# Kernel tuning notes

Hardware: AMD Instinct MI355X
Metric: run time of the kernel (lower is better)

Reference implementation:

```python
import jax, jax.numpy as jnp
import numpy as np

HEADS = 4
NEG_SLOPE = 0.2  # PyG GATConv default
LN_EPS = 1e-5


def setup_inputs() -> dict:
    key = jax.random.key(0)
    ks = jax.random.split(key, 12)
    N, D, E = 30000, 128, 480000
    s = 1.0 / np.sqrt(D)
    return {
        "x": jax.random.normal(ks[0], (N, D), dtype=jnp.float32),
        "edge_index": jax.random.randint(ks[1], (2, E), 0, N, dtype=jnp.int64),
        "W_gat": jax.random.normal(ks[2], (HEADS, D, D), dtype=jnp.float32) * s,
        "att_src": jax.random.normal(ks[3], (HEADS, D), dtype=jnp.float32) * s,
        "att_dst": jax.random.normal(ks[4], (HEADS, D), dtype=jnp.float32) * s,
        "b_gat": jnp.zeros((D,), dtype=jnp.float32),
        "W_gcn": jax.random.normal(ks[5], (D, D), dtype=jnp.float32) * s,
        "b_gcn": jnp.zeros((D,), dtype=jnp.float32),
        "W_gate": jax.random.normal(ks[6], (2 * D, 2), dtype=jnp.float32) * (1.0 / np.sqrt(2 * D)),
        "b_gate": jnp.zeros((2,), dtype=jnp.float32),
        "gamma": jnp.ones((D,), dtype=jnp.float32),
        "beta": jnp.zeros((D,), dtype=jnp.float32),
    }


def reference(x, edge_index, W_gat, att_src, att_dst, b_gat, W_gcn, b_gcn,
              W_gate, b_gate, gamma, beta):
    N, D = x.shape
    # Both PyG GATConv and GCNConv add self-loops by default.
    loops = jnp.arange(N, dtype=edge_index.dtype)
    src = jnp.concatenate([edge_index[0], loops])  # message source j
    dst = jnp.concatenate([edge_index[1], loops])  # message target i

    # ---- GATConv (heads=4, concat=False -> mean over heads), eval (no dropout) ----
    xh = jnp.einsum('nd,hdf->nhf', x, W_gat)            # [N, H, D]
    a_s = jnp.einsum('nhf,hf->nh', xh, att_src)         # [N, H]
    a_d = jnp.einsum('nhf,hf->nh', xh, att_dst)         # [N, H]
    e = jax.nn.leaky_relu(a_s[src] + a_d[dst], NEG_SLOPE)  # [E', H]
    # segment softmax over incoming edges of each destination node
    m = jax.ops.segment_max(e, dst, num_segments=N)     # every node has a self-loop
    alpha = jnp.exp(e - m[dst])
    denom = jax.ops.segment_sum(alpha, dst, num_segments=N)
    alpha = alpha / denom[dst]                          # [E', H]
    # aggregate per head (fixed small loop keeps peak memory at E*D per head)
    gat_acc = jnp.zeros((N, D), dtype=x.dtype)
    for h in range(HEADS):
        msg = alpha[:, h:h + 1] * xh[:, h, :][src]      # [E', D]
        gat_acc = gat_acc + jax.ops.segment_sum(msg, dst, num_segments=N)
    gat_out = gat_acc / HEADS + b_gat

    xg = x @ W_gcn                                      # [N, D]
    deg = jax.ops.segment_sum(jnp.ones_like(src, dtype=x.dtype), dst, num_segments=N)
    dinv = jnp.where(deg > 0, jax.lax.rsqrt(deg), 0.0)
    coef = dinv[src] * dinv[dst]                        # [E']
    gcn_out = jax.ops.segment_sum(coef[:, None] * xg[src], dst, num_segments=N) + b_gcn

    # ---- gated fusion + residual + LayerNorm ----
    gate = jax.nn.softmax(jnp.concatenate([gat_out, gcn_out], axis=-1) @ W_gate + b_gate, axis=-1)
    fused = gate[:, 0:1] * gat_out + gate[:, 1:2] * gcn_out
    h = fused + gat_out
    mu = jnp.mean(h, axis=-1, keepdims=True)
    var = jnp.mean((h - mu) ** 2, axis=-1, keepdims=True)
    return (h - mu) * jax.lax.rsqrt(var + LN_EPS) * gamma + beta
```

## Files before the change

kernel.cpp:

```cpp
#include <hip/hip_runtime.h>
#include <hip/hip_bf16.h>

#define D 128
#define NH 4
#define NEG_SLOPE 0.2f
#define LN_EPS 1e-5f

typedef __attribute__((ext_vector_type(4))) float f32x4;
typedef __attribute__((ext_vector_type(8))) short bf16x8;

__device__ __forceinline__ float bf2f(unsigned short u) {
  union { unsigned int i; float f; } c; c.i = ((unsigned int)u) << 16; return c.f;
}
__device__ __forceinline__ unsigned short f2bf(float f) {
  union { float f; unsigned int i; } c; c.f = f;
  unsigned int r = c.i + 0x7FFFu + ((c.i >> 16) & 1u);
  return (unsigned short)(r >> 16);
}

__global__ __launch_bounds__(128) void k_prep(
    const float* __restrict__ Wgat, const float* __restrict__ Wgcn,
    const float* __restrict__ att_src, const float* __restrict__ att_dst,
    unsigned short* __restrict__ Wt2g, unsigned short* __restrict__ Wt2c,
    float* __restrict__ wtil_s, float* __restrict__ wtil_d)
{
  int c = blockIdx.x, t = threadIdx.x;
  if (c < 128) {
    #pragma unroll
    for (int i = 0; i < 4; ++i) {
      int k = t + i * 128;
      int h = k >> 7, kk = k & 127;
      Wt2g[c * 512 + k] = f2bf(Wgat[((size_t)h * D + kk) * D + c]);
    }
  } else if (c < 256) {
    int cc = c - 128;
    Wt2c[cc * 128 + t] = f2bf(Wgcn[(size_t)t * D + cc]);
  } else {
    int b2 = c - 256;
    int h = b2 >> 1, which = b2 & 1;
    const float* av = (which ? att_dst : att_src) + h * D;
    const float* Wrow = Wgat + ((size_t)h * D + t) * D;
    float s = 0.f;
    for (int f = 0; f < D; ++f) s += Wrow[f] * av[f];
    (which ? wtil_d : wtil_s)[h * D + t] = s;
  }
}

__global__ __launch_bounds__(256) void k_xb(
    const float* __restrict__ x,
    const float* __restrict__ wtil_s, const float* __restrict__ wtil_d,
    unsigned short* __restrict__ xb, float* __restrict__ a_s, float* __restrict__ a_d,
    int* __restrict__ deg, int N)
{
  const int w = threadIdx.x >> 6, l = threadIdx.x & 63;
  const int n = blockIdx.x * 4 + w;
  if (n >= N) return;
  if (l == 0) deg[n] = 0;
  float2 xv = ((const float2*)(x + (size_t)n * D))[l];
  ushort2 p; p.x = f2bf(xv.x); p.y = f2bf(xv.y);
  *(ushort2*)(xb + (size_t)n * D + 2 * l) = p;
  float s0 = xv.x * wtil_s[2*l]       + xv.y * wtil_s[2*l+1];
  float s1 = xv.x * wtil_s[D+2*l]     + xv.y * wtil_s[D+2*l+1];
  float s2 = xv.x * wtil_s[2*D+2*l]   + xv.y * wtil_s[2*D+2*l+1];
  float s3 = xv.x * wtil_s[3*D+2*l]   + xv.y * wtil_s[3*D+2*l+1];
  float d0 = xv.x * wtil_d[2*l]       + xv.y * wtil_d[2*l+1];
  float d1 = xv.x * wtil_d[D+2*l]     + xv.y * wtil_d[D+2*l+1];
  float d2 = xv.x * wtil_d[2*D+2*l]   + xv.y * wtil_d[2*D+2*l+1];
  float d3 = xv.x * wtil_d[3*D+2*l]   + xv.y * wtil_d[3*D+2*l+1];
  #pragma unroll
  for (int off = 32; off; off >>= 1) {
    s0 += __shfl_xor(s0, off); s1 += __shfl_xor(s1, off);
    s2 += __shfl_xor(s2, off); s3 += __shfl_xor(s3, off);
    d0 += __shfl_xor(d0, off); d1 += __shfl_xor(d1, off);
    d2 += __shfl_xor(d2, off); d3 += __shfl_xor(d3, off);
  }
  if (l == 0) {
    ((float4*)a_s)[n] = make_float4(s0, s1, s2, s3);
    ((float4*)a_d)[n] = make_float4(d0, d1, d2, d3);
  }
}

__global__ void k_deg(const int* __restrict__ ei, int E, int N, int* __restrict__ deg)
{
  int e = blockIdx.x * blockDim.x + threadIdx.x;
  if (e >= E + N) return;
  int dst = (e < E) ? ei[E + e] : (e - E);
  atomicAdd(&deg[dst], 1);
}

__global__ void k_scan1(const int* __restrict__ deg, int N, int* __restrict__ bsum)
{
  __shared__ int s[256];
  int t = threadIdx.x;
  int i = blockIdx.x * 256 + t;
  s[t] = (i < N) ? deg[i] : 0;
  __syncthreads();
  for (int off = 128; off; off >>= 1) {
    if (t < off) s[t] += s[t + off];
    __syncthreads();
  }
  if (t == 0) bsum[blockIdx.x] = s[0];
}

__global__ void k_scan2(int* __restrict__ bsum, int nb)
{
  __shared__ int s[128];
  int t = threadIdx.x;
  int v = (t < nb) ? bsum[t] : 0;
  s[t] = v; __syncthreads();
  for (int off = 1; off < 128; off <<= 1) {
    int xv = (t >= off) ? s[t - off] : 0;
    __syncthreads();
    s[t] += xv;
    __syncthreads();
  }
  if (t < nb) bsum[t] = s[t] - v;
}

__global__ void k_scan3(const int* __restrict__ deg, const int* __restrict__ bsum,
                        int N, int Et, int* __restrict__ row_ptr,
                        int* __restrict__ cursor, float* __restrict__ dinv)
{
  __shared__ int s[256];
  int t = threadIdx.x;
  int i = blockIdx.x * 256 + t;
  int v = (i < N) ? deg[i] : 0;
  s[t] = v; __syncthreads();
  for (int off = 1; off < 256; off <<= 1) {
    int xv = (t >= off) ? s[t - off] : 0;
    __syncthreads();
    s[t] += xv;
    __syncthreads();
  }
  if (i < N) {
    int excl = s[t] - v + bsum[blockIdx.x];
    row_ptr[i] = excl;
    cursor[i] = excl;
    dinv[i] = rsqrtf((float)v);
  }
  if (i == 0) row_ptr[N] = Et;
}

__global__ void k_fill(const int* __restrict__ ei, int E, int N,
                       int* __restrict__ cursor, int* __restrict__ col_src)
{
  int e = blockIdx.x * blockDim.x + threadIdx.x;
  if (e >= E + N) return;
  int src, dst;
  if (e < E) { src = ei[e]; dst = ei[E + e]; }
  else       { src = e - E; dst = src; }
  int pos = atomicAdd(&cursor[dst], 1);
  col_src[pos] = src;
}

__global__ __launch_bounds__(256) void k_agg2(
    const unsigned short* __restrict__ xb,
    const float* __restrict__ a_s, const float* __restrict__ a_d,
    const int* __restrict__ row_ptr, const int* __restrict__ col_src,
    const float* __restrict__ dinv,
    unsigned short* __restrict__ UV, int N)
{
  __shared__ float4 sh_al[8][33];
  __shared__ int    sh_src[8][33];
  __shared__ float  sh_cf[8][33];
  const int hw = threadIdx.x >> 5, lh = threadIdx.x & 31;
  const int n = blockIdx.x * 8 + hw;
  if (n >= N) return;
  const int start = row_ptr[n], end = row_ptr[n + 1];
  const float4 adn = ((const float4*)a_d)[n];

  float den0 = 0.f, den1 = 0.f, den2 = 0.f, den3 = 0.f;
  float ug[4][4] = {};
  float vg[4] = {};

  for (int base = start; base < end; base += 32) {
    const int cnt = min(32, end - base);
    if (lh < cnt) {
      int s = col_src[base + lh];
      float4 as4 = ((const float4*)a_s)[s];
      float e0 = as4.x + adn.x; e0 = (e0 >= 0.f) ? e0 : NEG_SLOPE * e0;
      float e1 = as4.y + adn.y; e1 = (e1 >= 0.f) ? e1 : NEG_SLOPE * e1;
      float e2 = as4.z + adn.z; e2 = (e2 >= 0.f) ? e2 : NEG_SLOPE * e2;
      float e3 = as4.w + adn.w; e3 = (e3 >= 0.f) ? e3 : NEG_SLOPE * e3;
      float x0 = __expf(e0), x1 = __expf(e1), x2 = __expf(e2), x3 = __expf(e3);
      den0 += x0; den1 += x1; den2 += x2; den3 += x3;
      sh_al[hw][lh] = make_float4(x0, x1, x2, x3);
      sh_src[hw][lh] = s;
      sh_cf[hw][lh] = dinv[s];
    }
    if (lh == 0) {
      sh_al[hw][cnt] = make_float4(0.f, 0.f, 0.f, 0.f);
      sh_src[hw][cnt] = 0;
      sh_cf[hw][cnt] = 0.f;
    }
    for (int j = 0; j < cnt; j += 2) {
      float4 alA = sh_al[hw][j];     int sA = sh_src[hw][j];     float cfA = sh_cf[hw][j];
      float4 alB = sh_al[hw][j + 1]; int sB = sh_src[hw][j + 1]; float cfB = sh_cf[hw][j + 1];
      ushort4 xA = *(const ushort4*)(xb + ((size_t)sA << 7) + (lh << 2));
      ushort4 xB = *(const ushort4*)(xb + ((size_t)sB << 7) + (lh << 2));
      float fa[4] = {bf2f(xA.x), bf2f(xA.y), bf2f(xA.z), bf2f(xA.w)};
      float fb[4] = {bf2f(xB.x), bf2f(xB.y), bf2f(xB.z), bf2f(xB.w)};
      float aA[4] = {alA.x, alA.y, alA.z, alA.w};
      float aB[4] = {alB.x, alB.y, alB.z, alB.w};
      #pragma unroll
      for (int h = 0; h < 4; ++h)
        #pragma unroll
        for (int d = 0; d < 4; ++d)
          ug[h][d] += aA[h] * fa[d] + aB[h] * fb[d];
      #pragma unroll
      for (int d = 0; d < 4; ++d)
        vg[d] += cfA * fa[d] + cfB * fb[d];
    }
  }

  #pragma unroll
  for (int off = 16; off; off >>= 1) {
    den0 += __shfl_xor(den0, off); den1 += __shfl_xor(den1, off);
    den2 += __shfl_xor(den2, off); den3 += __shfl_xor(den3, off);
  }
  const float r[4] = {1.f / den0, 1.f / den1, 1.f / den2, 1.f / den3};
  const float dn = dinv[n];
  unsigned short* uvp = UV + (size_t)n * 640;
  #pragma unroll
  for (int h = 0; h < 4; ++h) {
    ushort4 u;
    u.x = f2bf(ug[h][0] * r[h]); u.y = f2bf(ug[h][1] * r[h]);
    u.z = f2bf(ug[h][2] * r[h]); u.w = f2bf(ug[h][3] * r[h]);
    *(ushort4*)(uvp + h * 128 + 4 * lh) = u;
  }
  ushort4 v4;
  v4.x = f2bf(vg[0] * dn); v4.y = f2bf(vg[1] * dn);
  v4.z = f2bf(vg[2] * dn); v4.w = f2bf(vg[3] * dn);
  *(ushort4*)(uvp + 512 + 4 * lh) = v4;
}

__global__ __launch_bounds__(256) void k_gemm3(
    const unsigned short* __restrict__ UV,
    const unsigned short* __restrict__ Wt2g, const unsigned short* __restrict__ Wt2c,
    const float* __restrict__ b_gat, const float* __restrict__ b_gcn,
    const float* __restrict__ W_gate, const float* __restrict__ b_gate,
    const float* __restrict__ gamma, const float* __restrict__ beta,
    float* __restrict__ out, int N)
{
  __shared__ unsigned short As[128 * 128];
  __shared__ unsigned short Bs[128 * 128];
  __shared__ float ec[8][128];
  const int t = threadIdx.x;
  const int m0 = blockIdx.x * 128;

  {
    int idx = t * 4;
    #pragma unroll
    for (int i = 0; i < 4; ++i) {
      int arr = (idx + i) >> 7, c = (idx + i) & 127;
      float v;
      switch (arr) {
        case 0: v = b_gat[c]; break;
        case 1: v = b_gcn[c]; break;
        case 2: v = W_gate[2 * c]; break;
        case 3: v = W_gate[2 * c + 1]; break;
        case 4: v = W_gate[256 + 2 * c]; break;
        case 5: v = W_gate[256 + 2 * c + 1]; break;
        case 6: v = gamma[c]; break;
        default: v = beta[c]; break;
      }
      ec[arr][c] = v;
    }
  }

  const int w = t >> 6, l = t & 63;
  const int lrow = l & 15, lk = l >> 4;

  f32x4 accg[2][8], accc[2][8];
  #pragma unroll
  for (int m = 0; m < 2; ++m)
    #pragma unroll
    for (int n = 0; n < 8; ++n) {
      accg[m][n] = (f32x4){0.f, 0.f, 0.f, 0.f};
      accc[m][n] = (f32x4){0.f, 0.f, 0.f, 0.f};
    }

  for (int kc = 0; kc < 5; ++kc) {
    const int abase = (kc < 4) ? kc * 128 : 512;
    __syncthreads();
    #pragma unroll
    for (int i = 0; i < 8; ++i) {
      int g = i * 256 + t;
      int row = g >> 4, kb = g & 15;
      int gr = m0 + row;
      uint4 v = make_uint4(0u, 0u, 0u, 0u);
      if (gr < N) v = *(const uint4*)(UV + (size_t)gr * 640 + abase + kb * 8);
      *(uint4*)&As[row * 128 + ((kb ^ (row & 7)) << 3)] = v;
    }
    #pragma unroll
    for (int i = 0; i < 8; ++i) {
      int g = i * 256 + t;
      int col = g >> 4, kb = g & 15;
      uint4 v = (kc < 4)
        ? *(const uint4*)(Wt2g + (size_t)col * 512 + kc * 128 + kb * 8)
        : *(const uint4*)(Wt2c + (size_t)col * 128 + kb * 8);
      *(uint4*)&Bs[col * 128 + ((kb ^ (col & 7)) << 3)] = v;
    }
    __syncthreads();
    if (kc < 4) {
      #pragma unroll
      for (int ks = 0; ks < 4; ++ks) {
        int kb = ks * 4 + lk;
        bf16x8 a[2], b[8];
        #pragma unroll
        for (int m = 0; m < 2; ++m) {
          int row = w * 32 + m * 16 + lrow;
          a[m] = *(const bf16x8*)&As[row * 128 + ((kb ^ (row & 7)) << 3)];
        }
        #pragma unroll
        for (int n = 0; n < 8; ++n) {
          int col = n * 16 + lrow;
          b[n] = *(const bf16x8*)&Bs[col * 128 + ((kb ^ (col & 7)) << 3)];
        }
        #pragma unroll
        for (int m = 0; m < 2; ++m)
          #pragma unroll
          for (int n = 0; n < 8; ++n)
            accg[m][n] = __builtin_amdgcn_mfma_f32_16x16x32_bf16(a[m], b[n], accg[m][n], 0, 0, 0);
      }
    } else {
      #pragma unroll
      for (int ks = 0; ks < 4; ++ks) {
        int kb = ks * 4 + lk;
        bf16x8 a[2], b[8];
        #pragma unroll
        for (int m = 0; m < 2; ++m) {
          int row = w * 32 + m * 16 + lrow;
          a[m] = *(const bf16x8*)&As[row * 128 + ((kb ^ (row & 7)) << 3)];
        }
        #pragma unroll
        for (int n = 0; n < 8; ++n) {
          int col = n * 16 + lrow;
          b[n] = *(const bf16x8*)&Bs[col * 128 + ((kb ^ (col & 7)) << 3)];
        }
        #pragma unroll
        for (int m = 0; m < 2; ++m)
          #pragma unroll
          for (int n = 0; n < 8; ++n)
            accc[m][n] = __builtin_amdgcn_mfma_f32_16x16x32_bf16(a[m], b[n], accc[m][n], 0, 0, 0);
      }
    }
  }

  const float bg0 = b_gate[0], bg1 = b_gate[1];
  #pragma unroll
  for (int m = 0; m < 2; ++m) {
    #pragma unroll
    for (int j = 0; j < 4; ++j) {
      const int r = m0 + w * 32 + m * 16 + lk * 4 + j;
      float ga[8], gc[8];
      float z0 = 0.f, z1 = 0.f;
      #pragma unroll
      for (int n = 0; n < 8; ++n) {
        int c = n * 16 + lrow;
        ga[n] = accg[m][n][j] * 0.25f + ec[0][c];
        gc[n] = accc[m][n][j] + ec[1][c];
        z0 += ga[n] * ec[2][c] + gc[n] * ec[4][c];
        z1 += ga[n] * ec[3][c] + gc[n] * ec[5][c];
      }
      #pragma unroll
      for (int off = 8; off; off >>= 1) { z0 += __shfl_xor(z0, off); z1 += __shfl_xor(z1, off); }
      z0 += bg0; z1 += bg1;
      float mz = fmaxf(z0, z1);
      float e0 = __expf(z0 - mz), e1 = __expf(z1 - mz);
      float inv = 1.f / (e0 + e1);
      float w0 = e0 * inv, w1 = e1 * inv;
      float h[8], ss = 0.f;
      #pragma unroll
      for (int n = 0; n < 8; ++n) { h[n] = (1.f + w0) * ga[n] + w1 * gc[n]; ss += h[n]; }
      #pragma unroll
      for (int off = 8; off; off >>= 1) ss += __shfl_xor(ss, off);
      float mu = ss * (1.f / 128.f);
      float vs = 0.f;
      #pragma unroll
      for (int n = 0; n < 8; ++n) { h[n] -= mu; vs += h[n] * h[n]; }
      #pragma unroll
      for (int off = 8; off; off >>= 1) vs += __shfl_xor(vs, off);
      float rstd = rsqrtf(vs * (1.f / 128.f) + LN_EPS);
      if (r < N) {
        #pragma unroll
        for (int n = 0; n < 8; ++n) {
          int c = n * 16 + lrow;
          out[(size_t)r * 128 + c] = h[n] * rstd * ec[6][c] + ec[7][c];
        }
      }
    }
  }
}

extern "C" void kernel_launch(void* const* d_in, const int* in_sizes, int n_in,
                              void* d_out, int out_size, void* d_ws, size_t ws_size,
                              hipStream_t stream)
{
  const float* x       = (const float*)d_in[0];
  const int*   ei      = (const int*)d_in[1];
  const float* Wgat    = (const float*)d_in[2];
  const float* att_src = (const float*)d_in[3];
  const float* att_dst = (const float*)d_in[4];
  const float* b_gat   = (const float*)d_in[5];
  const float* Wgcn    = (const float*)d_in[6];
  const float* b_gcn   = (const float*)d_in[7];
  const float* W_gate  = (const float*)d_in[8];
  const float* b_gate  = (const float*)d_in[9];
  const float* gamma   = (const float*)d_in[10];
  const float* beta    = (const float*)d_in[11];
  float* out = (float*)d_out;

  const int N  = in_sizes[0] / D;
  const int E  = in_sizes[1] / 2;
  const int Et = E + N;

  char* p = (char*)d_ws;
  unsigned short* xb   = (unsigned short*)p; p += (size_t)N * D * 2;
  unsigned short* UV   = (unsigned short*)p; p += (size_t)N * 640 * 2;
  unsigned short* Wt2g = (unsigned short*)p; p += (size_t)128 * 512 * 2;
  unsigned short* Wt2c = (unsigned short*)p; p += (size_t)128 * 128 * 2;
  float* wtil_s  = (float*)p; p += 512 * 4;
  float* wtil_d  = (float*)p; p += 512 * 4;
  float* a_s     = (float*)p; p += (size_t)N * NH * 4;
  float* a_d     = (float*)p; p += (size_t)N * NH * 4;
  float* dinv    = (float*)p; p += (size_t)N * 4;
  int* deg       = (int*)p;   p += (size_t)N * 4;
  int* row_ptr   = (int*)p;   p += (size_t)(N + 1) * 4;
  int* cursor    = (int*)p;   p += (size_t)N * 4;
  int* col_src   = (int*)p;   p += (size_t)Et * 4;
  int* bsum      = (int*)p;   p += 1024;

  k_prep<<<264, 128, 0, stream>>>(Wgat, Wgcn, att_src, att_dst,
                                   Wt2g, Wt2c, wtil_s, wtil_d);
  k_xb<<<(N + 3) / 4, 256, 0, stream>>>(x, wtil_s, wtil_d, xb, a_s, a_d, deg, N);
  k_deg<<<(Et + 255) / 256, 256, 0, stream>>>(ei, E, N, deg);
  int nb = (N + 255) / 256;
  k_scan1<<<nb, 256, 0, stream>>>(deg, N, bsum);
  k_scan2<<<1, 128, 0, stream>>>(bsum, nb);
  k_scan3<<<nb, 256, 0, stream>>>(deg, bsum, N, Et, row_ptr, cursor, dinv);
  k_fill<<<(Et + 255) / 256, 256, 0, stream>>>(ei, E, N, cursor, col_src);
  k_agg2<<<(N + 7) / 8, 256, 0, stream>>>(xb, a_s, a_d, row_ptr, col_src, dinv, UV, N);
  k_gemm3<<<(N + 127) / 128, 256, 0, stream>>>(UV, Wt2g, Wt2c, b_gat, b_gcn,
                                                W_gate, b_gate, gamma, beta, out, N);
  (void)n_in; (void)out_size; (void)ws_size;
}
```

Measured before the change: 145.4 us.

## Merge degree count into node kernel and halve GEMM row tile

```diff
diff --git a/kernel.cpp b/kernel.cpp
--- a/kernel.cpp
+++ b/kernel.cpp
@@ -22,7 +22,8 @@
     const float* __restrict__ Wgat, const float* __restrict__ Wgcn,
     const float* __restrict__ att_src, const float* __restrict__ att_dst,
     unsigned short* __restrict__ Wt2g, unsigned short* __restrict__ Wt2c,
-    float* __restrict__ wtil_s, float* __restrict__ wtil_d)
+    float* __restrict__ wtil_s, float* __restrict__ wtil_d,
+    int* __restrict__ deg, int N)
 {
   int c = blockIdx.x, t = threadIdx.x;
   if (c < 128) {
@@ -35,7 +36,7 @@
   } else if (c < 256) {
     int cc = c - 128;
     Wt2c[cc * 128 + t] = f2bf(Wgcn[(size_t)t * D + cc]);
-  } else {
+  } else if (c < 264) {
     int b2 = c - 256;
     int h = b2 >> 1, which = b2 & 1;
     const float* av = (which ? att_dst : att_src) + h * D;
@@ -43,19 +44,30 @@
     float s = 0.f;
     for (int f = 0; f < D; ++f) s += Wrow[f] * av[f];
     (which ? wtil_d : wtil_s)[h * D + t] = s;
-  }
-}
-
-__global__ __launch_bounds__(256) void k_xb(
+  } else {
+    int i = (c - 264) * 128 + t;
+    if (i < N) deg[i] = 0;
+  }
+}
+
+__global__ __launch_bounds__(256) void k_xb_deg(
     const float* __restrict__ x,
     const float* __restrict__ wtil_s, const float* __restrict__ wtil_d,
     unsigned short* __restrict__ xb, float* __restrict__ a_s, float* __restrict__ a_d,
-    int* __restrict__ deg, int N)
-{
+    const int* __restrict__ ei, int* __restrict__ deg,
+    int N, int E, int NBN)
+{
+  if ((int)blockIdx.x >= NBN) {
+    int e = (blockIdx.x - NBN) * 256 + threadIdx.x;
+    if (e < E + N) {
+      int dst = (e < E) ? ei[E + e] : (e - E);
+      atomicAdd(&deg[dst], 1);
+    }
+    return;
+  }
   const int w = threadIdx.x >> 6, l = threadIdx.x & 63;
   const int n = blockIdx.x * 4 + w;
   if (n >= N) return;
-  if (l == 0) deg[n] = 0;
   float2 xv = ((const float2*)(x + (size_t)n * D))[l];
   ushort2 p; p.x = f2bf(xv.x); p.y = f2bf(xv.y);
   *(ushort2*)(xb + (size_t)n * D + 2 * l) = p;
@@ -80,14 +92,6 @@
   }
 }
 
-__global__ void k_deg(const int* __restrict__ ei, int E, int N, int* __restrict__ deg)
-{
-  int e = blockIdx.x * blockDim.x + threadIdx.x;
-  if (e >= E + N) return;
-  int dst = (e < E) ? ei[E + e] : (e - E);
-  atomicAdd(&deg[dst], 1);
-}
-
 __global__ void k_scan1(const int* __restrict__ deg, int N, int* __restrict__ bsum)
 {
   __shared__ int s[256];
@@ -242,11 +246,11 @@
     const float* __restrict__ gamma, const float* __restrict__ beta,
     float* __restrict__ out, int N)
 {
-  __shared__ unsigned short As[128 * 128];
+  __shared__ unsigned short As[64 * 128];
   __shared__ unsigned short Bs[128 * 128];
   __shared__ float ec[8][128];
   const int t = threadIdx.x;
-  const int m0 = blockIdx.x * 128;
+  const int m0 = blockIdx.x * 64;
 
   {
     int idx = t * 4;
@@ -270,21 +274,20 @@
 
   const int w = t >> 6, l = t & 63;
   const int lrow = l & 15, lk = l >> 4;
-
-  f32x4 accg[2][8], accc[2][8];
+  const int arow = w * 16 + lrow;
+
+  f32x4 accg[8], accc[8];
   #pragma unroll
-  for (int m = 0; m < 2; ++m)
-    #pragma unroll
-    for (int n = 0; n < 8; ++n) {
-      accg[m][n] = (f32x4){0.f, 0.f, 0.f, 0.f};
-      accc[m][n] = (f32x4){0.f, 0.f, 0.f, 0.f};
-    }
+  for (int n = 0; n < 8; ++n) {
+    accg[n] = (f32x4){0.f, 0.f, 0.f, 0.f};
+    accc[n] = (f32x4){0.f, 0.f, 0.f, 0.f};
+  }
 
   for (int kc = 0; kc < 5; ++kc) {
     const int abase = (kc < 4) ? kc * 128 : 512;
     __syncthreads();
     #pragma unroll
-    for (int i = 0; i < 8; ++i) {
+    for (int i = 0; i < 4; ++i) {
       int g = i * 256 + t;
       int row = g >> 4, kb = g & 15;
       int gr = m0 + row;
@@ -302,92 +305,58 @@
       *(uint4*)&Bs[col * 128 + ((kb ^ (col & 7)) << 3)] = v;
     }
     __syncthreads();
-    if (kc < 4) {
+    f32x4* acc = (kc < 4) ? accg : accc;
+    #pragma unroll
+    for (int ks = 0; ks < 4; ++ks) {
+      int kb = ks * 4 + lk;
+      bf16x8 a = *(const bf16x8*)&As[arow * 128 + ((kb ^ (arow & 7)) << 3)];
       #pragma unroll
-      for (int ks = 0; ks < 4; ++ks) {
-        int kb = ks * 4 + lk;
-        bf16x8 a[2], b[8];
-        #pragma unroll
-        for (int m = 0; m < 2; ++m) {
-          int row = w * 32 + m * 16 + lrow;
-          a[m] = *(const bf16x8*)&As[row * 128 + ((kb ^ (row & 7)) << 3)];
-        }
-        #pragma unroll
-        for (int n = 0; n < 8; ++n) {
-          int col = n * 16 + lrow;
-          b[n] = *(const bf16x8*)&Bs[col * 128 + ((kb ^ (col & 7)) << 3)];
-        }
-        #pragma unroll
-        for (int m = 0; m < 2; ++m)
-          #pragma unroll
-          for (int n = 0; n < 8; ++n)
-            accg[m][n] = __builtin_amdgcn_mfma_f32_16x16x32_bf16(a[m], b[n], accg[m][n], 0, 0, 0);
-      }
-    } else {
-      #pragma unroll
-      for (int ks = 0; ks < 4; ++ks) {
-        int kb = ks * 4 + lk;
-        bf16x8 a[2], b[8];
-        #pragma unroll
-        for (int m = 0; m < 2; ++m) {
-          int row = w * 32 + m * 16 + lrow;
-          a[m] = *(const bf16x8*)&As[row * 128 + ((kb ^ (row & 7)) << 3)];
-        }
-        #pragma unroll
-        for (int n = 0; n < 8; ++n) {
-          int col = n * 16 + lrow;
-          b[n] = *(const bf16x8*)&Bs[col * 128 + ((kb ^ (col & 7)) << 3)];
-        }
-        #pragma unroll
-        for (int m = 0; m < 2; ++m)
-          #pragma unroll
-          for (int n = 0; n < 8; ++n)
-            accc[m][n] = __builtin_amdgcn_mfma_f32_16x16x32_bf16(a[m], b[n], accc[m][n], 0, 0, 0);
+      for (int n = 0; n < 8; ++n) {
+        int col = n * 16 + lrow;
+        bf16x8 b = *(const bf16x8*)&Bs[col * 128 + ((kb ^ (col & 7)) << 3)];
+        acc[n] = __builtin_amdgcn_mfma_f32_16x16x32_bf16(a, b, acc[n], 0, 0, 0);
       }
     }
   }
 
   const float bg0 = b_gate[0], bg1 = b_gate[1];
   #pragma unroll
-  for (int m = 0; m < 2; ++m) {
-    #pragma unroll
-    for (int j = 0; j < 4; ++j) {
-      const int r = m0 + w * 32 + m * 16 + lk * 4 + j;
-      float ga[8], gc[8];
-      float z0 = 0.f, z1 = 0.f;
+  for (int j = 0; j < 4; ++j) {
+    const int r = m0 + w * 16 + lk * 4 + j;
+    float ga[8], gc[8];
+    float z0 = 0.f, z1 = 0.f;
+    #pragma unroll
+    for (int n = 0; n < 8; ++n) {
+      int c = n * 16 + lrow;
+      ga[n] = accg[n][j] * 0.25f + ec[0][c];
+      gc[n] = accc[n][j] + ec[1][c];
+      z0 += ga[n] * ec[2][c] + gc[n] * ec[4][c];
+      z1 += ga[n] * ec[3][c] + gc[n] * ec[5][c];
+    }
+    #pragma unroll
+    for (int off = 8; off; off >>= 1) { z0 += __shfl_xor(z0, off); z1 += __shfl_xor(z1, off); }
+    z0 += bg0; z1 += bg1;
+    float mz = fmaxf(z0, z1);
+    float e0 = __expf(z0 - mz), e1 = __expf(z1 - mz);
+    float inv = 1.f / (e0 + e1);
+    float w0 = e0 * inv, w1 = e1 * inv;
+    float h[8], ss = 0.f;
+    #pragma unroll
+    for (int n = 0; n < 8; ++n) { h[n] = (1.f + w0) * ga[n] + w1 * gc[n]; ss += h[n]; }
+    #pragma unroll
+    for (int off = 8; off; off >>= 1) ss += __shfl_xor(ss, off);
+    float mu = ss * (1.f / 128.f);
+    float vs = 0.f;
+    #pragma unroll
+    for (int n = 0; n < 8; ++n) { h[n] -= mu; vs += h[n] * h[n]; }
+    #pragma unroll
+    for (int off = 8; off; off >>= 1) vs += __shfl_xor(vs, off);
+    float rstd = rsqrtf(vs * (1.f / 128.f) + LN_EPS);
+    if (r < N) {
       #pragma unroll
       for (int n = 0; n < 8; ++n) {
         int c = n * 16 + lrow;
-        ga[n] = accg[m][n][j] * 0.25f + ec[0][c];
-        gc[n] = accc[m][n][j] + ec[1][c];
-        z0 += ga[n] * ec[2][c] + gc[n] * ec[4][c];
-        z1 += ga[n] * ec[3][c] + gc[n] * ec[5][c];
-      }
-      #pragma unroll
-      for (int off = 8; off; off >>= 1) { z0 += __shfl_xor(z0, off); z1 += __shfl_xor(z1, off); }
-      z0 += bg0; z1 += bg1;
-      float mz = fmaxf(z0, z1);
-      float e0 = __expf(z0 - mz), e1 = __expf(z1 - mz);
-      float inv = 1.f / (e0 + e1);
-      float w0 = e0 * inv, w1 = e1 * inv;
-      float h[8], ss = 0.f;
-      #pragma unroll
-      for (int n = 0; n < 8; ++n) { h[n] = (1.f + w0) * ga[n] + w1 * gc[n]; ss += h[n]; }
-      #pragma unroll
-      for (int off = 8; off; off >>= 1) ss += __shfl_xor(ss, off);
-      float mu = ss * (1.f / 128.f);
-      float vs = 0.f;
-      #pragma unroll
-      for (int n = 0; n < 8; ++n) { h[n] -= mu; vs += h[n] * h[n]; }
-      #pragma unroll
-      for (int off = 8; off; off >>= 1) vs += __shfl_xor(vs, off);
-      float rstd = rsqrtf(vs * (1.f / 128.f) + LN_EPS);
-      if (r < N) {
-        #pragma unroll
-        for (int n = 0; n < 8; ++n) {
-          int c = n * 16 + lrow;
-          out[(size_t)r * 128 + c] = h[n] * rstd * ec[6][c] + ec[7][c];
-        }
+        out[(size_t)r * 128 + c] = h[n] * rstd * ec[6][c] + ec[7][c];
       }
     }
   }
@@ -431,17 +400,20 @@
   int* col_src   = (int*)p;   p += (size_t)Et * 4;
   int* bsum      = (int*)p;   p += 1024;
 
-  k_prep<<<264, 128, 0, stream>>>(Wgat, Wgcn, att_src, att_dst,
-                                   Wt2g, Wt2c, wtil_s, wtil_d);
-  k_xb<<<(N + 3) / 4, 256, 0, stream>>>(x, wtil_s, wtil_d, xb, a_s, a_d, deg, N);
-  k_deg<<<(Et + 255) / 256, 256, 0, stream>>>(ei, E, N, deg);
+  const int NBN = (N + 3) / 4;
+  const int NBE = (Et + 255) / 256;
+
+  k_prep<<<264 + (N + 127) / 128, 128, 0, stream>>>(
+      Wgat, Wgcn, att_src, att_dst, Wt2g, Wt2c, wtil_s, wtil_d, deg, N);
+  k_xb_deg<<<NBN + NBE, 256, 0, stream>>>(x, wtil_s, wtil_d, xb, a_s, a_d,
+                                           ei, deg, N, E, NBN);
   int nb = (N + 255) / 256;
   k_scan1<<<nb, 256, 0, stream>>>(deg, N, bsum);
   k_scan2<<<1, 128, 0, stream>>>(bsum, nb);
   k_scan3<<<nb, 256, 0, stream>>>(deg, bsum, N, Et, row_ptr, cursor, dinv);
   k_fill<<<(Et + 255) / 256, 256, 0, stream>>>(ei, E, N, cursor, col_src);
   k_agg2<<<(N + 7) / 8, 256, 0, stream>>>(xb, a_s, a_d, row_ptr, col_src, dinv, UV, N);
-  k_gemm3<<<(N + 127) / 128, 256, 0, stream>>>(UV, Wt2g, Wt2c, b_gat, b_gcn,
-                                                W_gate, b_gate, gamma, beta, out, N);
+  k_gemm3<<<(N + 63) / 64, 256, 0, stream>>>(UV, Wt2g, Wt2c, b_gat, b_gcn,
+                                              W_gate, b_gate, gamma, beta, out, N);
   (void)n_in; (void)out_size; (void)ws_size;
 }
```

Result: faster. 131.9 us (-9.3%).
